# Kernel tuning notes

Hardware: AMD Instinct MI355X
Metric: run time of the kernel (lower is better)

Reference implementation:

```python
import jax, jax.numpy as jnp
import numpy as np


def _gru_cell(x, h, w_ih, w_hh, b_ih, b_hh):
    # PyTorch GRU cell, gate order (r, z, n)
    gi = x @ w_ih.T + b_ih          # [B, 3*d_dec]
    gh = h @ w_hh.T + b_hh          # [B, 3*d_dec]
    i_r, i_z, i_n = jnp.split(gi, 3, axis=-1)
    h_r, h_z, h_n = jnp.split(gh, 3, axis=-1)
    r = jax.nn.sigmoid(i_r + h_r)
    z = jax.nn.sigmoid(i_z + h_z)
    n = jnp.tanh(i_n + r * h_n)
    return (1.0 - z) * n + z * h


def setup_inputs() -> dict:
    key = jax.random.key(0)
    ks = jax.random.split(key, 6)
    D_VOCAB, D_EMB, D_DEC = 32000, 512, 1024
    s = 0.02
    return {
        "embs": jax.random.normal(ks[0], (D_VOCAB, D_EMB), jnp.float32) * s,
        "init": jax.random.normal(ks[1], (1, D_DEC), jnp.float32) * s,
        "w_ih": jax.random.normal(ks[2], (3 * D_DEC, D_EMB), jnp.float32) * s,
        "w_hh": jax.random.normal(ks[3], (3 * D_DEC, D_DEC), jnp.float32) * s,
        "b_ih": jnp.zeros((3 * D_DEC,), jnp.float32),
        "b_hh": jnp.zeros((3 * D_DEC,), jnp.float32),
        "W_out": jax.random.normal(ks[4], (D_VOCAB, D_DEC), jnp.float32) * s,
        "b_out": jnp.zeros((D_VOCAB,), jnp.float32),
        "bos_idx": 1,
        "batch_size": 64,
        "num_steps": 64,
    }


def reference(embs, init, w_ih, w_hh, b_ih, b_hh, W_out, b_out, bos_idx, batch_size, num_steps):
    d_dec = init.shape[1]
    state = jnp.broadcast_to(init, (batch_size, d_dec))          # self.init.expand(B, -1)
    word = jnp.broadcast_to(embs[bos_idx], (batch_size, embs.shape[1]))  # BOS embedding

    def step(carry, _):
        state, word = carry
        state = _gru_cell(word, state, w_ih, w_hh, b_ih, b_hh)   # single GRU step
        logits = state @ W_out.T + b_out                          # [B, V]
        pred = jnp.argmax(logits, axis=-1)                        # sample_func = argmax
        next_word = embs[pred]                                    # embed sampled token
        return (state, next_word), (logits, pred)

    (_, _), (logits, preds) = jax.lax.scan(step, (state, word), None, length=num_steps)
    logits = jnp.swapaxes(logits, 0, 1)  # [B, T, V]
    preds = jnp.swapaxes(preds, 0, 1)    # [B, T]
    return logits, preds
```

## Files before the change

kernel.cpp:

```cpp
#include <hip/hip_runtime.h>
#include <stdint.h>

#define D_EMB 512
#define D_DEC 1024
#define VOCAB 32000
#define BATCH 64
#define STEPS 64

struct Ws {
    float h[2][D_DEC];
    float logits[VOCAB];
    unsigned long long slot[STEPS];
};

__device__ __forceinline__ unsigned long long pack_lv(float f, int v) {
    unsigned u = __float_as_uint(f);
    unsigned key = (u & 0x80000000u) ? ~u : (u | 0x80000000u);
    return ((unsigned long long)key << 32) | (unsigned)(0xFFFFFFFFu - (unsigned)v);
}
__device__ __forceinline__ int unpack_v(unsigned long long p) {
    return (int)(0xFFFFFFFFu - (unsigned)(p & 0xFFFFFFFFu));
}

__global__ __launch_bounds__(256) void k_gates(
    const float* __restrict__ embs, const float* __restrict__ init,
    const float* __restrict__ w_ih, const float* __restrict__ w_hh,
    const float* __restrict__ b_ih, const float* __restrict__ b_hh,
    const int* __restrict__ bos_idx,
    float* __restrict__ out_logits, float* __restrict__ out_preds,
    Ws* __restrict__ ws, int t)
{
    const int lane = threadIdx.x & 63;
    const int gtid = blockIdx.x * blockDim.x + threadIdx.x;
    const int nthr = gridDim.x * blockDim.x;
    const int wid  = gtid >> 6;

    int pred_prev;
    if (t == 0) pred_prev = *bos_idx;
    else        pred_prev = unpack_v(ws->slot[t - 1]);

    if (t > 0) {
        const float4* lb = (const float4*)ws->logits;
        float4* ob = (float4*)out_logits;
        const int VQ = VOCAB / 4;
        for (int idx = gtid; idx < BATCH * VQ; idx += nthr) {
            int b = idx / VQ;
            int c = idx - b * VQ;
            ob[(size_t)b * (STEPS * (size_t)VQ) + (size_t)(t - 1) * VQ + c] = lb[c];
        }
        if (gtid < BATCH) out_preds[gtid * STEPS + (t - 1)] = (float)pred_prev;
    } else {
        if (gtid < STEPS) ws->slot[gtid] = 0ull;
    }

    if (t >= STEPS) return;

    const int j = wid;
    if (j >= D_DEC) return;

    const float* hprev = (t == 0) ? init : ws->h[(t + 1) & 1];
    const float* x     = embs + (size_t)pred_prev * D_EMB;

    const float4* x4   = (const float4*)x;
    const float4* h4   = (const float4*)hprev;
    const float4* wih4 = (const float4*)w_ih;
    const float4* whh4 = (const float4*)w_hh;

    float s_ir = 0.f, s_iz = 0.f, s_in = 0.f;
    float s_hr = 0.f, s_hz = 0.f, s_hn = 0.f;

    #pragma unroll
    for (int k0 = 0; k0 < 2; ++k0) {
        int k = k0 * 64 + lane;
        float4 xv = x4[k];
        float4 a = wih4[(size_t)j * 128 + k];
        float4 b = wih4[(size_t)(j + D_DEC) * 128 + k];
        float4 c = wih4[(size_t)(j + 2 * D_DEC) * 128 + k];
        s_ir += a.x * xv.x + a.y * xv.y + a.z * xv.z + a.w * xv.w;
        s_iz += b.x * xv.x + b.y * xv.y + b.z * xv.z + b.w * xv.w;
        s_in += c.x * xv.x + c.y * xv.y + c.z * xv.z + c.w * xv.w;
    }
    #pragma unroll
    for (int k0 = 0; k0 < 4; ++k0) {
        int k = k0 * 64 + lane;
        float4 hv = h4[k];
        float4 a = whh4[(size_t)j * 256 + k];
        float4 b = whh4[(size_t)(j + D_DEC) * 256 + k];
        float4 c = whh4[(size_t)(j + 2 * D_DEC) * 256 + k];
        s_hr += a.x * hv.x + a.y * hv.y + a.z * hv.z + a.w * hv.w;
        s_hz += b.x * hv.x + b.y * hv.y + b.z * hv.z + b.w * hv.w;
        s_hn += c.x * hv.x + c.y * hv.y + c.z * hv.z + c.w * hv.w;
    }

    #pragma unroll
    for (int off = 32; off > 0; off >>= 1) {
        s_ir += __shfl_down(s_ir, off, 64);
        s_iz += __shfl_down(s_iz, off, 64);
        s_in += __shfl_down(s_in, off, 64);
        s_hr += __shfl_down(s_hr, off, 64);
        s_hz += __shfl_down(s_hz, off, 64);
        s_hn += __shfl_down(s_hn, off, 64);
    }

    if (lane == 0) {
        float ir = s_ir + b_ih[j];
        float iz = s_iz + b_ih[j + D_DEC];
        float in_ = s_in + b_ih[j + 2 * D_DEC];
        float hr = s_hr + b_hh[j];
        float hz = s_hz + b_hh[j + D_DEC];
        float hn = s_hn + b_hh[j + 2 * D_DEC];
        float r = 1.f / (1.f + expf(-(ir + hr)));
        float z = 1.f / (1.f + expf(-(iz + hz)));
        float n = tanhf(in_ + r * hn);
        ws->h[t & 1][j] = (1.f - z) * n + z * hprev[j];
    }
}

__global__ __launch_bounds__(256) void k_logits(
    const float* __restrict__ W_out, const float* __restrict__ b_out,
    Ws* __restrict__ ws, int t)
{
    const int lane = threadIdx.x & 63;
    const int widx = threadIdx.x >> 6;
    const int wid  = blockIdx.x * 4 + widx;
    const int nw   = gridDim.x * 4;

    const float4* h4 = (const float4*)ws->h[t & 1];
    float4 hr[4];
    #pragma unroll
    for (int k = 0; k < 4; ++k) hr[k] = h4[k * 64 + lane];

    const float4* W4 = (const float4*)W_out;
    unsigned long long best = 0ull;

    for (int v = wid; v < VOCAB; v += nw) {
        const float4* row = W4 + (size_t)v * 256;
        float s = 0.f;
        #pragma unroll
        for (int k = 0; k < 4; ++k) {
            float4 w = row[k * 64 + lane];
            s += w.x * hr[k].x + w.y * hr[k].y + w.z * hr[k].z + w.w * hr[k].w;
        }
        #pragma unroll
        for (int off = 32; off > 0; off >>= 1) s += __shfl_down(s, off, 64);
        if (lane == 0) {
            float logit = s + b_out[v];
            ws->logits[v] = logit;
            unsigned long long p = pack_lv(logit, v);
            if (p > best) best = p;
        }
    }

    __shared__ unsigned long long sb[4];
    if (lane == 0) sb[widx] = best;
    __syncthreads();
    if (threadIdx.x == 0) {
        unsigned long long b = sb[0];
        #pragma unroll
        for (int i = 1; i < 4; ++i) if (sb[i] > b) b = sb[i];
        atomicMax(&ws->slot[t], b);
    }
}

extern "C" void kernel_launch(void* const* d_in, const int* in_sizes, int n_in,
                              void* d_out, int out_size, void* d_ws, size_t ws_size,
                              hipStream_t stream) {
    const float* embs  = (const float*)d_in[0];
    const float* init  = (const float*)d_in[1];
    const float* w_ih  = (const float*)d_in[2];
    const float* w_hh  = (const float*)d_in[3];
    const float* b_ih  = (const float*)d_in[4];
    const float* b_hh  = (const float*)d_in[5];
    const float* W_out = (const float*)d_in[6];
    const float* b_out = (const float*)d_in[7];
    const int*   bos   = (const int*)d_in[8];

    float* out_logits = (float*)d_out;
    float* out_preds  = out_logits + (size_t)BATCH * STEPS * VOCAB;

    Ws* ws = (Ws*)d_ws;

    for (int t = 0; t <= STEPS; ++t) {
        hipLaunchKernelGGL(k_gates, dim3(256), dim3(256), 0, stream,
                           embs, init, w_ih, w_hh, b_ih, b_hh, bos,
                           out_logits, out_preds, ws, t);
        if (t < STEPS) {
            hipLaunchKernelGGL(k_logits, dim3(512), dim3(256), 0, stream,
                               W_out, b_out, ws, t);
        }
    }
}
```

Measured before the change: 2.717 ms.

## Move hidden-state GEMV into logits kernel and replace atomic argmax with per-block bests

Computes the h@W_hh gate projection for the next step inside the logits kernel, using a dedicated set of blocks that run concurrently with the vocabulary GEMV. This removes the serial W_hh pass from the gates kernel. The atomicMax slot is replaced by per-block best values that the next gates kernel reduces, each wave now processes four rows with h staged in LDS, and the logits copy uses nontemporal stores. The costs are a redundant reduction of about 936 block bests in every gates block and a changed grid size.

After: 2.873 ms. 5.7% more time.

```diff
diff --git a/kernel.cpp b/kernel.cpp
--- a/kernel.cpp
+++ b/kernel.cpp
@@ -7,10 +7,18 @@
 #define BATCH 64
 #define STEPS 64
 
+#define LOG_BLOCKS 1024
+#define GH_BLOCKS  88
+#define VOC_BLOCKS (LOG_BLOCKS - GH_BLOCKS)
+#define NBB        VOC_BLOCKS
+
+typedef float f32x4 __attribute__((ext_vector_type(4)));
+
 struct Ws {
     float h[2][D_DEC];
+    float gh[3 * D_DEC];
     float logits[VOCAB];
-    unsigned long long slot[STEPS];
+    unsigned long long bbest[NBB];
 };
 
 __device__ __forceinline__ unsigned long long pack_lv(float f, int v) {
@@ -30,27 +38,50 @@
     float* __restrict__ out_logits, float* __restrict__ out_preds,
     Ws* __restrict__ ws, int t)
 {
-    const int lane = threadIdx.x & 63;
-    const int gtid = blockIdx.x * blockDim.x + threadIdx.x;
-    const int nthr = gridDim.x * blockDim.x;
+    const int tid  = threadIdx.x;
+    const int lane = tid & 63;
+    const int widx = tid >> 6;
+    const int gtid = blockIdx.x * 256 + tid;
+    const int nthr = gridDim.x * 256;
     const int wid  = gtid >> 6;
 
-    int pred_prev;
-    if (t == 0) pred_prev = *bos_idx;
-    else        pred_prev = unpack_v(ws->slot[t - 1]);
+    __shared__ unsigned long long sb[4];
 
     if (t > 0) {
-        const float4* lb = (const float4*)ws->logits;
-        float4* ob = (float4*)out_logits;
+        unsigned long long bb = 0ull;
+        for (int i = tid; i < NBB; i += 256) {
+            unsigned long long p = ws->bbest[i];
+            if (p > bb) bb = p;
+        }
+        #pragma unroll
+        for (int off = 32; off > 0; off >>= 1) {
+            unsigned long long o = __shfl_down(bb, off, 64);
+            if (o > bb) bb = o;
+        }
+        if (lane == 0) sb[widx] = bb;
+
+        const f32x4* lb = (const f32x4*)ws->logits;
+        f32x4* ob = (f32x4*)out_logits;
         const int VQ = VOCAB / 4;
         for (int idx = gtid; idx < BATCH * VQ; idx += nthr) {
             int b = idx / VQ;
             int c = idx - b * VQ;
-            ob[(size_t)b * (STEPS * (size_t)VQ) + (size_t)(t - 1) * VQ + c] = lb[c];
-        }
-        if (gtid < BATCH) out_preds[gtid * STEPS + (t - 1)] = (float)pred_prev;
+            __builtin_nontemporal_store(
+                lb[c], &ob[(size_t)b * (STEPS * (size_t)VQ) + (size_t)(t - 1) * VQ + c]);
+        }
+    }
+
+    int pred;
+    if (t == 0) {
+        pred = *bos_idx;
     } else {
-        if (gtid < STEPS) ws->slot[gtid] = 0ull;
+        __syncthreads();
+        unsigned long long m = sb[0];
+        #pragma unroll
+        for (int i = 1; i < 4; ++i) if (sb[i] > m) m = sb[i];
+        pred = unpack_v(m);
+        if (gtid < BATCH)
+            __builtin_nontemporal_store((float)pred, &out_preds[gtid * STEPS + (t - 1)]);
     }
 
     if (t >= STEPS) return;
@@ -59,16 +90,10 @@
     if (j >= D_DEC) return;
 
     const float* hprev = (t == 0) ? init : ws->h[(t + 1) & 1];
-    const float* x     = embs + (size_t)pred_prev * D_EMB;
-
-    const float4* x4   = (const float4*)x;
-    const float4* h4   = (const float4*)hprev;
+    const float4* x4   = (const float4*)(embs + (size_t)pred * D_EMB);
     const float4* wih4 = (const float4*)w_ih;
-    const float4* whh4 = (const float4*)w_hh;
 
     float s_ir = 0.f, s_iz = 0.f, s_in = 0.f;
-    float s_hr = 0.f, s_hz = 0.f, s_hn = 0.f;
-
     #pragma unroll
     for (int k0 = 0; k0 < 2; ++k0) {
         int k = k0 * 64 + lane;
@@ -80,16 +105,22 @@
         s_iz += b.x * xv.x + b.y * xv.y + b.z * xv.z + b.w * xv.w;
         s_in += c.x * xv.x + c.y * xv.y + c.z * xv.z + c.w * xv.w;
     }
-    #pragma unroll
-    for (int k0 = 0; k0 < 4; ++k0) {
-        int k = k0 * 64 + lane;
-        float4 hv = h4[k];
-        float4 a = whh4[(size_t)j * 256 + k];
-        float4 b = whh4[(size_t)(j + D_DEC) * 256 + k];
-        float4 c = whh4[(size_t)(j + 2 * D_DEC) * 256 + k];
-        s_hr += a.x * hv.x + a.y * hv.y + a.z * hv.z + a.w * hv.w;
-        s_hz += b.x * hv.x + b.y * hv.y + b.z * hv.z + b.w * hv.w;
-        s_hn += c.x * hv.x + c.y * hv.y + c.z * hv.z + c.w * hv.w;
+
+    float s_hr = 0.f, s_hz = 0.f, s_hn = 0.f;
+    if (t == 0) {
+        const float4* h4   = (const float4*)hprev;
+        const float4* whh4 = (const float4*)w_hh;
+        #pragma unroll
+        for (int k0 = 0; k0 < 4; ++k0) {
+            int k = k0 * 64 + lane;
+            float4 hv = h4[k];
+            float4 a = whh4[(size_t)j * 256 + k];
+            float4 b = whh4[(size_t)(j + D_DEC) * 256 + k];
+            float4 c = whh4[(size_t)(j + 2 * D_DEC) * 256 + k];
+            s_hr += a.x * hv.x + a.y * hv.y + a.z * hv.z + a.w * hv.w;
+            s_hz += b.x * hv.x + b.y * hv.y + b.z * hv.z + b.w * hv.w;
+            s_hn += c.x * hv.x + c.y * hv.y + c.z * hv.z + c.w * hv.w;
+        }
     }
 
     #pragma unroll
@@ -97,53 +128,95 @@
         s_ir += __shfl_down(s_ir, off, 64);
         s_iz += __shfl_down(s_iz, off, 64);
         s_in += __shfl_down(s_in, off, 64);
-        s_hr += __shfl_down(s_hr, off, 64);
-        s_hz += __shfl_down(s_hz, off, 64);
-        s_hn += __shfl_down(s_hn, off, 64);
+        if (t == 0) {
+            s_hr += __shfl_down(s_hr, off, 64);
+            s_hz += __shfl_down(s_hz, off, 64);
+            s_hn += __shfl_down(s_hn, off, 64);
+        }
     }
 
     if (lane == 0) {
-        float ir = s_ir + b_ih[j];
-        float iz = s_iz + b_ih[j + D_DEC];
+        float ir  = s_ir + b_ih[j];
+        float iz  = s_iz + b_ih[j + D_DEC];
         float in_ = s_in + b_ih[j + 2 * D_DEC];
-        float hr = s_hr + b_hh[j];
-        float hz = s_hz + b_hh[j + D_DEC];
-        float hn = s_hn + b_hh[j + 2 * D_DEC];
-        float r = 1.f / (1.f + expf(-(ir + hr)));
-        float z = 1.f / (1.f + expf(-(iz + hz)));
-        float n = tanhf(in_ + r * hn);
+        float hr_, hz_, hn_;
+        if (t == 0) {
+            hr_ = s_hr + b_hh[j];
+            hz_ = s_hz + b_hh[j + D_DEC];
+            hn_ = s_hn + b_hh[j + 2 * D_DEC];
+        } else {
+            hr_ = ws->gh[j];
+            hz_ = ws->gh[j + D_DEC];
+            hn_ = ws->gh[j + 2 * D_DEC];
+        }
+        float r = 1.f / (1.f + expf(-(ir + hr_)));
+        float z = 1.f / (1.f + expf(-(iz + hz_)));
+        float n = tanhf(in_ + r * hn_);
         ws->h[t & 1][j] = (1.f - z) * n + z * hprev[j];
     }
 }
 
-__global__ __launch_bounds__(256) void k_logits(
+__global__ __launch_bounds__(256, 4) void k_logits(
     const float* __restrict__ W_out, const float* __restrict__ b_out,
+    const float* __restrict__ w_hh, const float* __restrict__ b_hh,
     Ws* __restrict__ ws, int t)
 {
-    const int lane = threadIdx.x & 63;
-    const int widx = threadIdx.x >> 6;
-    const int wid  = blockIdx.x * 4 + widx;
-    const int nw   = gridDim.x * 4;
+    const int tid  = threadIdx.x;
+    const int lane = tid & 63;
+    const int widx = tid >> 6;
+    const int sub  = lane & 15;
+    const int grp  = lane >> 4;
+
+    __shared__ float4 sh[256];
+    __shared__ unsigned long long sb[4];
 
     const float4* h4 = (const float4*)ws->h[t & 1];
-    float4 hr[4];
-    #pragma unroll
-    for (int k = 0; k < 4; ++k) hr[k] = h4[k * 64 + lane];
-
+    sh[tid] = h4[tid];
+    __syncthreads();
+
+    if (blockIdx.x < GH_BLOCKS) {
+        const int gw  = blockIdx.x * 4 + widx;
+        const int ngw = GH_BLOCKS * 4;
+        const float4* whh4 = (const float4*)w_hh;
+        for (int g0 = gw * 4; g0 < 3 * D_DEC; g0 += ngw * 4) {
+            const int g = g0 + grp;
+            const float4* row = whh4 + (size_t)g * 256;
+            float s = 0.f;
+            #pragma unroll
+            for (int k = 0; k < 16; ++k) {
+                float4 w  = row[sub + k * 16];
+                float4 hv = sh[sub + k * 16];
+                s += w.x * hv.x + w.y * hv.y + w.z * hv.z + w.w * hv.w;
+            }
+            s += __shfl_xor(s, 1, 64);
+            s += __shfl_xor(s, 2, 64);
+            s += __shfl_xor(s, 4, 64);
+            s += __shfl_xor(s, 8, 64);
+            if (sub == 0) ws->gh[g] = s + b_hh[g];
+        }
+        return;
+    }
+
+    const int vw  = (blockIdx.x - GH_BLOCKS) * 4 + widx;
+    const int nvw = VOC_BLOCKS * 4;
     const float4* W4 = (const float4*)W_out;
+
     unsigned long long best = 0ull;
-
-    for (int v = wid; v < VOCAB; v += nw) {
+    for (int v0 = vw * 4; v0 < VOCAB; v0 += nvw * 4) {
+        const int v = v0 + grp;
         const float4* row = W4 + (size_t)v * 256;
         float s = 0.f;
         #pragma unroll
-        for (int k = 0; k < 4; ++k) {
-            float4 w = row[k * 64 + lane];
-            s += w.x * hr[k].x + w.y * hr[k].y + w.z * hr[k].z + w.w * hr[k].w;
-        }
-        #pragma unroll
-        for (int off = 32; off > 0; off >>= 1) s += __shfl_down(s, off, 64);
-        if (lane == 0) {
+        for (int k = 0; k < 16; ++k) {
+            float4 w  = row[sub + k * 16];
+            float4 hv = sh[sub + k * 16];
+            s += w.x * hv.x + w.y * hv.y + w.z * hv.z + w.w * hv.w;
+        }
+        s += __shfl_xor(s, 1, 64);
+        s += __shfl_xor(s, 2, 64);
+        s += __shfl_xor(s, 4, 64);
+        s += __shfl_xor(s, 8, 64);
+        if (sub == 0) {
             float logit = s + b_out[v];
             ws->logits[v] = logit;
             unsigned long long p = pack_lv(logit, v);
@@ -151,14 +224,18 @@
         }
     }
 
-    __shared__ unsigned long long sb[4];
+    #pragma unroll
+    for (int off = 32; off > 0; off >>= 1) {
+        unsigned long long o = __shfl_down(best, off, 64);
+        if (o > best) best = o;
+    }
     if (lane == 0) sb[widx] = best;
     __syncthreads();
-    if (threadIdx.x == 0) {
-        unsigned long long b = sb[0];
-        #pragma unroll
-        for (int i = 1; i < 4; ++i) if (sb[i] > b) b = sb[i];
-        atomicMax(&ws->slot[t], b);
+    if (tid == 0) {
+        unsigned long long m = sb[0];
+        #pragma unroll
+        for (int i = 1; i < 4; ++i) if (sb[i] > m) m = sb[i];
+        ws->bbest[blockIdx.x - GH_BLOCKS] = m;
     }
 }
 
@@ -185,8 +262,8 @@
                            embs, init, w_ih, w_hh, b_ih, b_hh, bos,
                            out_logits, out_preds, ws, t);
         if (t < STEPS) {
-            hipLaunchKernelGGL(k_logits, dim3(512), dim3(256), 0, stream,
-                               W_out, b_out, ws, t);
-        }
-    }
-}
+            hipLaunchKernelGGL(k_logits, dim3(LOG_BLOCKS), dim3(256), 0, stream,
+                               W_out, b_out, w_hh, b_hh, ws, t);
+        }
+    }
+}
```
